# Optimization experiments

Measured on AMD Instinct MI355X. Metric: run time of the kernel, lower is better.

## Reference

```python
import jax, jax.numpy as jnp
import numpy as np

N_NODES = 10000
N_EDGES = 640000
D_IN = 128
D_OUT = 128


def setup_inputs() -> dict:
    key = jax.random.key(0)
    k1, k2, k3, k4 = jax.random.split(key, 4)
    x = jax.random.normal(k1, (N_NODES, D_IN), dtype=jnp.float32)
    # PyG GCNConv weight: [dim_out, dim_in] (glorot)
    W = jax.random.normal(k2, (D_OUT, D_IN), dtype=jnp.float32) * (1.0 / np.sqrt(D_IN))
    b = jnp.zeros((D_OUT,), dtype=jnp.float32)
    edge_weight = jax.random.uniform(k3, (N_EDGES,), dtype=jnp.float32)
    edge_index = jax.random.randint(k4, (2, N_EDGES), 0, N_NODES, dtype=jnp.int32)
    return {"x": x, "W": W, "b": b, "edge_weight": edge_weight, "edge_index": edge_index}


def reference(x, W, b, edge_weight, edge_index):
    N = x.shape[0]
    # --- add self loops (fill weight = 1.0), PyG default ---
    loops = jnp.arange(N, dtype=edge_index.dtype)
    src = jnp.concatenate([edge_index[0], loops])
    dst = jnp.concatenate([edge_index[1], loops])
    ew = jnp.concatenate([edge_weight, jnp.ones((N,), dtype=edge_weight.dtype)])
    # --- symmetric GCN normalization: deg from target index ---
    deg = jax.ops.segment_sum(ew, dst, num_segments=N)
    dinv = jnp.where(deg > 0, jax.lax.rsqrt(deg), 0.0)
    norm = dinv[src] * ew * dinv[dst]  # [E+N]
    # --- linear transform then gather-scale-scatter aggregation ---
    h = x @ W.T  # [N, D_OUT]
    msgs = h[src] * norm[:, None]  # [E+N, D_OUT]
    out = jax.ops.segment_sum(msgs, dst, num_segments=N)
    return out + b
```

## Files before the change

### kernel.cpp

```cpp
#include <hip/hip_runtime.h>

#define N_NODES 10000
#define N_EDGES 640000
#define D 128
#define CAP 128

typedef unsigned long long ull;
typedef unsigned short u16;
typedef unsigned int u32;

#define CHUNKS 128
#define EPC 5000
#define GEMM_NPB 32
#define GEMM_BLOCKS ((N_NODES + GEMM_NPB - 1) / GEMM_NPB)
#define SMEM_BYTES 80000
#define FRACM 0xffffffffffffull

__device__ __forceinline__ u16 f2bf(float f) {
    unsigned u = __float_as_uint(f);
    unsigned r = (u + 0x7fffu + ((u >> 16) & 1u)) >> 16;
    return (u16)r;
}


__global__ void __launch_bounds__(256, 2) k_hist_fill_gemm(
    const int* __restrict__ src, const int* __restrict__ dst,
    const float* __restrict__ ew, ull* __restrict__ gpacked,
    const float* __restrict__ x, const float* __restrict__ W,
    u16* __restrict__ h_bf, ull* __restrict__ csr)
{
    extern __shared__ char smem[];
    const int t = threadIdx.x;

    if (blockIdx.x < CHUNKS) {
        ull* hist = (ull*)smem;
        for (int i = t; i < N_NODES; i += 256) hist[i] = 0;
        __syncthreads();

        const int e0 = blockIdx.x * EPC;
        u32 dlr[20];
        #pragma unroll
        for (int i = 0; i < 20; ++i) {
            int idx = i * 256 + t;
            dlr[i] = 0xffffffffu;
            if (idx < EPC) {
                int e = e0 + idx;
                int d = dst[e];
                ull add = (1ull << 48) | (ull)(ew[e] * 4294967296.0f);
                ull old = atomicAdd(&hist[d], add);
                dlr[i] = ((u32)d << 7) | (u32)((old >> 48) & 127u);
            }
        }
        __syncthreads();

        for (int i = t; i < N_NODES; i += 256) {
            ull v = hist[i];
            if (v) {
                ull old = atomicAdd(&gpacked[i], v);
                hist[i] = old >> 48;
            }
        }
        __syncthreads();

        #pragma unroll
        for (int i = 0; i < 20; ++i) {
            if (dlr[i] != 0xffffffffu) {
                int e = e0 + i * 256 + t;
                int d = (int)(dlr[i] >> 7);
                int lr = (int)(dlr[i] & 127u);
                int slot = (int)(u32)hist[d] + lr;
                csr[(size_t)d * CAP + slot] =
                    ((ull)__float_as_uint(ew[e]) << 32) | (unsigned)src[e];
            }
        }
    } else {
        float* xs = (float*)smem;
        const int gb = blockIdx.x - CHUNKS;
        const int node0 = gb * GEMM_NPB;
        const int col = t & 127;
        const int half = t >> 7;

        #pragma unroll
        for (int r = 0; r < 16; ++r) {
            int row = half * 16 + r;
            int n = node0 + row;
            xs[row * D + col] = (n < N_NODES) ? x[n * D + col] : 0.0f;
        }
        __syncthreads();

        float acc[16];
        #pragma unroll
        for (int r = 0; r < 16; ++r) acc[r] = 0.0f;

        const float4* Wrow = (const float4*)&W[col * D];
        const float* xbase = &xs[half * 16 * D];
        for (int k4 = 0; k4 < D / 4; ++k4) {
            float4 w = Wrow[k4];
            int k = k4 * 4;
            #pragma unroll
            for (int r = 0; r < 16; ++r) {
                acc[r] += xbase[r * D + k + 0] * w.x;
                acc[r] += xbase[r * D + k + 1] * w.y;
                acc[r] += xbase[r * D + k + 2] * w.z;
                acc[r] += xbase[r * D + k + 3] * w.w;
            }
        }
        #pragma unroll
        for (int r = 0; r < 16; ++r) {
            int n = node0 + half * 16 + r;
            if (n < N_NODES) h_bf[n * D + col] = f2bf(acc[r]);
        }
    }
}


__global__ void k_agg(const ull* __restrict__ gpacked, const ull* __restrict__ csr,
                      const u16* __restrict__ h_bf, const float* __restrict__ b,
                      float* __restrict__ out) {
    const int n = blockIdx.x;
    const int tid = threadIdx.x;
    const int jj = tid >> 4;
    const int lane = tid & 15;
    __shared__ int   ssrc[CAP];
    __shared__ float snm[CAP];
    __shared__ float4 red[128][2];

    const ull gp = gpacked[n];
    const int deg = (int)(gp >> 48);
    const float dn = rsqrtf(1.0f + (float)(gp & FRACM) * 0x1p-32f);
    const ull* bucket = csr + (size_t)n * CAP;

    if (tid < deg) {
        ull v = bucket[tid];
        int s = (int)(unsigned)(v & 0xffffffffu);
        float w = __uint_as_float((u32)(v >> 32));
        ull gs = gpacked[s];
        float ds_ = rsqrtf(1.0f + (float)(gs & FRACM) * 0x1p-32f);
        ssrc[tid] = s;
        snm[tid] = ds_ * w * dn;
    }
    __syncthreads();

    float acc[8];
    #pragma unroll
    for (int k = 0; k < 8; ++k) acc[k] = 0.0f;

    for (int j = jj; j < deg; j += 8) {
        int s = ssrc[j];
        float nm = snm[j];
        union { float4 f4; unsigned u[4]; } uu;
        uu.f4 = *(const float4*)(h_bf + (size_t)s * D + lane * 8);
        #pragma unroll
        for (int k = 0; k < 4; ++k) {
            acc[2 * k]     += __uint_as_float(uu.u[k] << 16) * nm;
            acc[2 * k + 1] += __uint_as_float(uu.u[k] & 0xffff0000u) * nm;
        }
    }
    red[tid][0] = make_float4(acc[0], acc[1], acc[2], acc[3]);
    red[tid][1] = make_float4(acc[4], acc[5], acc[6], acc[7]);
    __syncthreads();

    if (tid < 16) {
        float r0[8];
        #pragma unroll
        for (int k = 0; k < 8; ++k) r0[k] = 0.0f;
        #pragma unroll
        for (int s = 0; s < 8; ++s) {
            float4 a = red[s * 16 + tid][0];
            float4 c = red[s * 16 + tid][1];
            r0[0] += a.x; r0[1] += a.y; r0[2] += a.z; r0[3] += a.w;
            r0[4] += c.x; r0[5] += c.y; r0[6] += c.z; r0[7] += c.w;
        }
        float s2 = dn * dn;
        union { float4 f4; unsigned u[4]; } hh;
        hh.f4 = *(const float4*)(h_bf + (size_t)n * D + tid * 8);
        float hv[8];
        #pragma unroll
        for (int k = 0; k < 4; ++k) {
            hv[2 * k]     = __uint_as_float(hh.u[k] << 16);
            hv[2 * k + 1] = __uint_as_float(hh.u[k] & 0xffff0000u);
        }
        const float4* b4 = (const float4*)(b + tid * 8);
        float4 b0 = b4[0], b1 = b4[1];
        float4 o0, o1;
        o0.x = r0[0] + hv[0] * s2 + b0.x;
        o0.y = r0[1] + hv[1] * s2 + b0.y;
        o0.z = r0[2] + hv[2] * s2 + b0.z;
        o0.w = r0[3] + hv[3] * s2 + b0.w;
        o1.x = r0[4] + hv[4] * s2 + b1.x;
        o1.y = r0[5] + hv[5] * s2 + b1.y;
        o1.z = r0[6] + hv[6] * s2 + b1.z;
        o1.w = r0[7] + hv[7] * s2 + b1.w;
        float4* o4 = (float4*)(out + (size_t)n * D + tid * 8);
        o4[0] = o0;
        o4[1] = o1;
    }
}


extern "C" void kernel_launch(void* const* d_in, const int* in_sizes, int n_in,
                              void* d_out, int out_size, void* d_ws, size_t ws_size,
                              hipStream_t stream) {
    const float* x  = (const float*)d_in[0];
    const float* W  = (const float*)d_in[1];
    const float* b  = (const float*)d_in[2];
    const float* ew = (const float*)d_in[3];
    const int* ei   = (const int*)d_in[4];
    const int* src = ei;
    const int* dst = ei + N_EDGES;
    float* out = (float*)d_out;

    char* ws = (char*)d_ws;
    ull*   gpacked = (ull*)(ws);
    u16*   h_bf    = (u16*)(ws + 80000);
    ull*   csr     = (ull*)(ws + 2640000);

    hipMemsetAsync(gpacked, 0, 80000, stream);
    k_hist_fill_gemm<<<CHUNKS + GEMM_BLOCKS, 256, SMEM_BYTES, stream>>>(
        src, dst, ew, gpacked, x, W, h_bf, csr);
    k_agg<<<N_NODES, 128, 0, stream>>>(gpacked, csr, h_bf, b, out);
}
```

Measured before the change: 122.8 us.

## Pack degree and CSR entries into 32-bit words and use wavefront-per-node aggregation

Degree count and weight sum now share one 32-bit word: an 8-bit count and a 24-bit fixed-point weight sum. CSR entries pack a quantized edge weight with a 14-bit source index, which halves the atomic width, the shared histogram and the CSR traffic. The aggregation kernel now maps one 64-lane wavefront to each node, with four nodes per block. It reduces with shuffles instead of shared memory and syncthreads, and computes per-edge norms inline. The trade-off is reduced precision of weights and degree sums, plus overflow risk if a node gets more than 255 in-edges or its weight sum exceeds the 24-bit fixed-point range.

```diff
diff --git a/kernel.cpp b/kernel.cpp
--- a/kernel.cpp
+++ b/kernel.cpp
@@ -13,8 +13,12 @@
 #define EPC 5000
 #define GEMM_NPB 32
 #define GEMM_BLOCKS ((N_NODES + GEMM_NPB - 1) / GEMM_NPB)
-#define SMEM_BYTES 80000
-#define FRACM 0xffffffffffffull
+#define SMEM_BYTES 40000
+#define EW_FX 131072.0f
+#define CNT_SH 24
+#define EW_MASK 0xffffffu
+#define EWQ_FX 262144.0f
+#define SRC_MASK 0x3fffu
 
 __device__ __forceinline__ u16 f2bf(float f) {
     unsigned u = __float_as_uint(f);
@@ -23,17 +27,17 @@
 }
 
 
-__global__ void __launch_bounds__(256, 2) k_hist_fill_gemm(
+__global__ void __launch_bounds__(256) k_hist_fill_gemm(
     const int* __restrict__ src, const int* __restrict__ dst,
-    const float* __restrict__ ew, ull* __restrict__ gpacked,
+    const float* __restrict__ ew, u32* __restrict__ gcw,
     const float* __restrict__ x, const float* __restrict__ W,
-    u16* __restrict__ h_bf, ull* __restrict__ csr)
+    u16* __restrict__ h_bf, u32* __restrict__ csr)
 {
     extern __shared__ char smem[];
     const int t = threadIdx.x;
 
     if (blockIdx.x < CHUNKS) {
-        ull* hist = (ull*)smem;
+        u32* hist = (u32*)smem;
         for (int i = t; i < N_NODES; i += 256) hist[i] = 0;
         __syncthreads();
 
@@ -46,18 +50,18 @@
             if (idx < EPC) {
                 int e = e0 + idx;
                 int d = dst[e];
-                ull add = (1ull << 48) | (ull)(ew[e] * 4294967296.0f);
-                ull old = atomicAdd(&hist[d], add);
-                dlr[i] = ((u32)d << 7) | (u32)((old >> 48) & 127u);
+                u32 add = (1u << CNT_SH) | (u32)(ew[e] * EW_FX + 0.5f);
+                u32 old = atomicAdd(&hist[d], add);
+                dlr[i] = ((u32)d << 7) | (old >> CNT_SH);
             }
         }
         __syncthreads();
 
         for (int i = t; i < N_NODES; i += 256) {
-            ull v = hist[i];
+            u32 v = hist[i];
             if (v) {
-                ull old = atomicAdd(&gpacked[i], v);
-                hist[i] = old >> 48;
+                u32 old = atomicAdd(&gcw[i], v);
+                hist[i] = old >> CNT_SH;
             }
         }
         __syncthreads();
@@ -68,9 +72,9 @@
                 int e = e0 + i * 256 + t;
                 int d = (int)(dlr[i] >> 7);
                 int lr = (int)(dlr[i] & 127u);
-                int slot = (int)(u32)hist[d] + lr;
-                csr[(size_t)d * CAP + slot] =
-                    ((ull)__float_as_uint(ew[e]) << 32) | (unsigned)src[e];
+                int slot = (int)hist[d] + lr;
+                u32 ewq = (u32)(ew[e] * EWQ_FX);
+                csr[(size_t)d * CAP + slot] = (ewq << 14) | (u32)src[e];
             }
         }
     } else {
@@ -114,84 +118,61 @@
 }
 
 
-__global__ void k_agg(const ull* __restrict__ gpacked, const ull* __restrict__ csr,
-                      const u16* __restrict__ h_bf, const float* __restrict__ b,
-                      float* __restrict__ out) {
-    const int n = blockIdx.x;
-    const int tid = threadIdx.x;
-    const int jj = tid >> 4;
-    const int lane = tid & 15;
-    __shared__ int   ssrc[CAP];
-    __shared__ float snm[CAP];
-    __shared__ float4 red[128][2];
-
-    const ull gp = gpacked[n];
-    const int deg = (int)(gp >> 48);
-    const float dn = rsqrtf(1.0f + (float)(gp & FRACM) * 0x1p-32f);
-    const ull* bucket = csr + (size_t)n * CAP;
-
-    if (tid < deg) {
-        ull v = bucket[tid];
-        int s = (int)(unsigned)(v & 0xffffffffu);
-        float w = __uint_as_float((u32)(v >> 32));
-        ull gs = gpacked[s];
-        float ds_ = rsqrtf(1.0f + (float)(gs & FRACM) * 0x1p-32f);
-        ssrc[tid] = s;
-        snm[tid] = ds_ * w * dn;
-    }
-    __syncthreads();
+__global__ void __launch_bounds__(256) k_agg(
+    const u32* __restrict__ gcw, const u32* __restrict__ csr,
+    const u16* __restrict__ h_bf, const float* __restrict__ bias,
+    float* __restrict__ out)
+{
+    const int n = blockIdx.x * 4 + (threadIdx.x >> 6);
+    const int lane = threadIdx.x & 63;
+    const int slice = lane >> 4;
+    const int li = lane & 15;
+
+    const u32 gn = gcw[n];
+    const int deg = (int)(gn >> CNT_SH);
+    const float dn = rsqrtf(1.0f + (float)(gn & EW_MASK) * (1.0f / EW_FX));
+    const u32* bucket = csr + (size_t)n * CAP;
 
     float acc[8];
     #pragma unroll
     for (int k = 0; k < 8; ++k) acc[k] = 0.0f;
 
-    for (int j = jj; j < deg; j += 8) {
-        int s = ssrc[j];
-        float nm = snm[j];
+    for (int j = slice; j < deg; j += 4) {
+        u32 v = bucket[j];
+        int s = (int)(v & SRC_MASK);
+        float w = (float)(v >> 14) * (1.0f / EWQ_FX);
+        u32 gs = gcw[s];
+        float ds_ = rsqrtf(1.0f + (float)(gs & EW_MASK) * (1.0f / EW_FX));
+        float nm = ds_ * w * dn;
         union { float4 f4; unsigned u[4]; } uu;
-        uu.f4 = *(const float4*)(h_bf + (size_t)s * D + lane * 8);
+        uu.f4 = *(const float4*)(h_bf + (size_t)s * D + li * 8);
         #pragma unroll
         for (int k = 0; k < 4; ++k) {
             acc[2 * k]     += __uint_as_float(uu.u[k] << 16) * nm;
             acc[2 * k + 1] += __uint_as_float(uu.u[k] & 0xffff0000u) * nm;
         }
     }
-    red[tid][0] = make_float4(acc[0], acc[1], acc[2], acc[3]);
-    red[tid][1] = make_float4(acc[4], acc[5], acc[6], acc[7]);
-    __syncthreads();
-
-    if (tid < 16) {
-        float r0[8];
-        #pragma unroll
-        for (int k = 0; k < 8; ++k) r0[k] = 0.0f;
-        #pragma unroll
-        for (int s = 0; s < 8; ++s) {
-            float4 a = red[s * 16 + tid][0];
-            float4 c = red[s * 16 + tid][1];
-            r0[0] += a.x; r0[1] += a.y; r0[2] += a.z; r0[3] += a.w;
-            r0[4] += c.x; r0[5] += c.y; r0[6] += c.z; r0[7] += c.w;
-        }
+    #pragma unroll
+    for (int k = 0; k < 8; ++k) {
+        acc[k] += __shfl_xor(acc[k], 16);
+        acc[k] += __shfl_xor(acc[k], 32);
+    }
+    if (slice == 0) {
         float s2 = dn * dn;
         union { float4 f4; unsigned u[4]; } hh;
-        hh.f4 = *(const float4*)(h_bf + (size_t)n * D + tid * 8);
-        float hv[8];
-        #pragma unroll
-        for (int k = 0; k < 4; ++k) {
-            hv[2 * k]     = __uint_as_float(hh.u[k] << 16);
-            hv[2 * k + 1] = __uint_as_float(hh.u[k] & 0xffff0000u);
-        }
-        const float4* b4 = (const float4*)(b + tid * 8);
+        hh.f4 = *(const float4*)(h_bf + (size_t)n * D + li * 8);
+        const float4* b4 = (const float4*)(bias + li * 8);
         float4 b0 = b4[0], b1 = b4[1];
         float4 o0, o1;
-        o0.x = r0[0] + hv[0] * s2 + b0.x;
-        o0.y = r0[1] + hv[1] * s2 + b0.y;
-        o0.z = r0[2] + hv[2] * s2 + b0.z;
-        o0.w = r0[3] + hv[3] * s2 + b0.w;
-        o1.x = r0[4] + hv[4] * s2 + b1.x;
-        o1.y = r0[5] + hv[5] * s2 + b1.y;
-        o1.z = r0[6] + hv[6] * s2 + b1.z;
-        o1.w = r0[7] + hv[7] * s2 + b1.w;
-        float4* o4 = (float4*)(out + (size_t)n * D + tid * 8);
+        o0.x = acc[0] + __uint_as_float(hh.u[0] << 16) * s2 + b0.x;
+        o0.y = acc[1] + __uint_as_float(hh.u[0] & 0xffff0000u) * s2 + b0.y;
+        o0.z = acc[2] + __uint_as_float(hh.u[1] << 16) * s2 + b0.z;
+        o0.w = acc[3] + __uint_as_float(hh.u[1] & 0xffff0000u) * s2 + b0.w;
+        o1.x = acc[4] + __uint_as_float(hh.u[2] << 16) * s2 + b1.x;
+        o1.y = acc[5] + __uint_as_float(hh.u[2] & 0xffff0000u) * s2 + b1.y;
+        o1.z = acc[6] + __uint_as_float(hh.u[3] << 16) * s2 + b1.z;
+        o1.w = acc[7] + __uint_as_float(hh.u[3] & 0xffff0000u) * s2 + b1.w;
+        float4* o4 = (float4*)(out + (size_t)n * D + li * 8);
         o4[0] = o0;
         o4[1] = o1;
     }
@@ -211,12 +192,12 @@
     float* out = (float*)d_out;
 
     char* ws = (char*)d_ws;
-    ull*   gpacked = (ull*)(ws);
-    u16*   h_bf    = (u16*)(ws + 80000);
-    ull*   csr     = (ull*)(ws + 2640000);
-
-    hipMemsetAsync(gpacked, 0, 80000, stream);
+    u32*   gcw  = (u32*)(ws);
+    u16*   h_bf = (u16*)(ws + 40000);
+    u32*   csr  = (u32*)(ws + 2600000);
+
+    hipMemsetAsync(gcw, 0, 40000, stream);
     k_hist_fill_gemm<<<CHUNKS + GEMM_BLOCKS, 256, SMEM_BYTES, stream>>>(
-        src, dst, ew, gpacked, x, W, h_bf, csr);
-    k_agg<<<N_NODES, 128, 0, stream>>>(gpacked, csr, h_bf, b, out);
-}
+        src, dst, ew, gcw, x, W, h_bf, csr);
+    k_agg<<<N_NODES / 4, 256, 0, stream>>>(gcw, csr, h_bf, b, out);
+}
```

Result: no change. 124.2 us (+1.1%).
